# Performance work log

Hardware: AMD Instinct MI355X
Metric: run time of the kernel (lower is better)

Reference implementation:

```python
import jax, jax.numpy as jnp
import numpy as np

N = 4_194_304
Q_DIM = W_DIM = V_DIM = U_DIM = 32
LATENT = 8


def setup_inputs() -> dict:
    key = jax.random.key(0)
    k1, k2 = jax.random.split(key)
    # coords in [0,1): guarantees index+1 stays in-bounds (matches quad4d assumptions)
    uvwq = jax.random.uniform(k1, (N, 4), dtype=jnp.float32)
    grid = jax.random.normal(k2, (Q_DIM, W_DIM, V_DIM, U_DIM, LATENT), dtype=jnp.float32)
    return {"uvwq": uvwq, "grid": grid}


def reference(uvwq, grid):
    # grid: [Q, W, V, U, L]; uvwq: [N, 4] with columns (u, v, w, q) in [0,1)
    Q, W, V, U, L = grid.shape
    scale = jnp.array([U - 1, V - 1, W - 1, Q - 1], dtype=uvwq.dtype)
    idxf = uvwq * scale                      # [N,4]
    idx = idxf.astype(jnp.int32)             # floor for non-negative coords
    frac = idxf - jnp.floor(idxf)
    a = frac[:, 0:1]  # alpha (u)
    b = frac[:, 1:2]  # beta  (v)
    g = frac[:, 2:3]  # gamma (w)
    d = frac[:, 3:4]  # delta (q)
    iu, iv, iw, iq = idx[:, 0], idx[:, 1], idx[:, 2], idx[:, 3]

    def corner(oq, ow, ov, ou):
        # 16-point gather: [N, L]
        return grid[iq + oq, iw + ow, iv + ov, iu + ou]

    def lerp(x0, x1, t):
        return x0 * (1 - t) + x1 * t

    # interpolate along u (alpha)
    x000 = lerp(corner(0, 0, 0, 0), corner(0, 0, 0, 1), a)
    x001 = lerp(corner(0, 0, 1, 0), corner(0, 0, 1, 1), a)
    x010 = lerp(corner(0, 1, 0, 0), corner(0, 1, 0, 1), a)
    x011 = lerp(corner(0, 1, 1, 0), corner(0, 1, 1, 1), a)
    x100 = lerp(corner(1, 0, 0, 0), corner(1, 0, 0, 1), a)
    x101 = lerp(corner(1, 0, 1, 0), corner(1, 0, 1, 1), a)
    x110 = lerp(corner(1, 1, 0, 0), corner(1, 1, 0, 1), a)
    x111 = lerp(corner(1, 1, 1, 0), corner(1, 1, 1, 1), a)
    # along v (beta)
    x00 = lerp(x000, x001, b)
    x01 = lerp(x010, x011, b)
    x10 = lerp(x100, x101, b)
    x11 = lerp(x110, x111, b)
    # along w (gamma)
    x0 = lerp(x00, x01, g)
    x1 = lerp(x10, x11, g)
    # along q (delta)
    return lerp(x0, x1, d)  # [N, L]
```

## Files before the change

kernel.cpp:

```cpp
#include <hip/hip_runtime.h>


typedef float v4f __attribute__((ext_vector_type(4)));

#define NB   256
#define PBLK 2048
#define PT   256

__device__ __forceinline__ int bucket_of(v4f p) {
    int iw = (int)(p.z * 31.0f);
    int iq = (int)(p.w * 31.0f);
    return (iq << 3) | (iw >> 2);
}

__global__ __launch_bounds__(PT) void k_hist(const v4f* __restrict__ uvwq,
                                             int* __restrict__ hist, int n) {
    __shared__ int lh[NB];
    int t = threadIdx.x;
    lh[t] = 0;
    __syncthreads();
    int base = blockIdx.x * PBLK;
#pragma unroll
    for (int j = 0; j < 8; ++j) {
        int i = base + j * PT + t;
        if (i < n) atomicAdd(&lh[bucket_of(uvwq[i])], 1);
    }
    __syncthreads();
    atomicAdd(&hist[t], lh[t]);
}

__global__ __launch_bounds__(NB) void k_scan(const int* __restrict__ hist,
                                             int* __restrict__ cursor) {
    __shared__ int sh[NB];
    int t = threadIdx.x;
    int v = hist[t];
    sh[t] = v;
    __syncthreads();
    for (int off = 1; off < NB; off <<= 1) {
        int x = (t >= off) ? sh[t - off] : 0;
        __syncthreads();
        sh[t] += x;
        __syncthreads();
    }
    cursor[t] = sh[t] - v;
}

__global__ __launch_bounds__(PT) void k_part(const v4f* __restrict__ uvwq,
                                             int* __restrict__ cursor,
                                             v4f* __restrict__ s_uvwq,
                                             int* __restrict__ s_idx, int n) {
    __shared__ int lh[NB], lbase[NB], lrsv[NB], lcnt[NB];
    __shared__ v4f sv[PBLK];
    __shared__ int si[PBLK];
    int t = threadIdx.x;
    int base = blockIdx.x * PBLK;

    lh[t] = 0;
    lcnt[t] = 0;
    __syncthreads();

    v4f p[8];
    int key[8];
#pragma unroll
    for (int j = 0; j < 8; ++j) {
        int i = base + j * PT + t;
        if (i < n) {
            p[j] = uvwq[i];
            key[j] = bucket_of(p[j]);
            atomicAdd(&lh[key[j]], 1);
        } else key[j] = -1;
    }
    __syncthreads();

    int v = lh[t];
    lbase[t] = v;
    __syncthreads();
    for (int off = 1; off < NB; off <<= 1) {
        int x = (t >= off) ? lbase[t - off] : 0;
        __syncthreads();
        lbase[t] += x;
        __syncthreads();
    }
    int excl = lbase[t] - v;
    __syncthreads();
    lbase[t] = excl;
    lrsv[t] = atomicAdd(&cursor[t], v);
    __syncthreads();

#pragma unroll
    for (int j = 0; j < 8; ++j) {
        if (key[j] >= 0) {
            int r = lbase[key[j]] + atomicAdd(&lcnt[key[j]], 1);
            sv[r] = p[j];
            si[r] = base + j * PT + t;
        }
    }
    __syncthreads();

    int cnt = min(PBLK, n - base);
#pragma unroll
    for (int j = 0; j < 8; ++j) {
        int s = j * PT + t;
        if (s < cnt) {
            v4f q = sv[s];
            int k = bucket_of(q);
            int gp = lrsv[k] + (s - lbase[k]);
            s_uvwq[gp] = q;
            s_idx[gp] = si[s];
        }
    }
}

__global__ __launch_bounds__(256) void k_interp(const v4f* __restrict__ s_uvwq,
                                                const int* __restrict__ s_idx,
                                                const float* __restrict__ grid,
                                                v4f* __restrict__ out, int n) {
    int nb = gridDim.x;
    int b = blockIdx.x;
    int swz = (nb & 7) ? b : (b & 7) * (nb >> 3) + (b >> 3);
    int g = swz * 256 + threadIdx.x;
    if (g >= n) return;

    int oi = s_idx[g];
    v4f p = s_uvwq[g];

    float fu = p.x * 31.0f, fv = p.y * 31.0f, fw = p.z * 31.0f, fq = p.w * 31.0f;
    int iu = (int)fu, iv = (int)fv, iw = (int)fw, iq = (int)fq;
    float a = fu - (float)iu;
    float bb = fv - (float)iv;
    float gg = fw - (float)iw;
    float d = fq - (float)iq;

    const float* cellbase = grid + ((((iq * 32 + iw) * 32) + iv) * 32 + iu) * 8;

    v4f c[8][4];
#pragma unroll
    for (int k = 0; k < 8; ++k) {
        const int oq = k >> 2, ow = (k >> 1) & 1, ov = k & 1;
        const v4f* cp = (const v4f*)(cellbase + oq * 262144 + ow * 8192 + ov * 256);
        c[k][0] = cp[0];
        c[k][1] = cp[1];
        c[k][2] = cp[2];
        c[k][3] = cp[3];
    }

    float xa[8][8];
#pragma unroll
    for (int k = 0; k < 8; ++k) {
        xa[k][0] = fmaf(a, c[k][2].x - c[k][0].x, c[k][0].x);
        xa[k][1] = fmaf(a, c[k][2].y - c[k][0].y, c[k][0].y);
        xa[k][2] = fmaf(a, c[k][2].z - c[k][0].z, c[k][0].z);
        xa[k][3] = fmaf(a, c[k][2].w - c[k][0].w, c[k][0].w);
        xa[k][4] = fmaf(a, c[k][3].x - c[k][1].x, c[k][1].x);
        xa[k][5] = fmaf(a, c[k][3].y - c[k][1].y, c[k][1].y);
        xa[k][6] = fmaf(a, c[k][3].z - c[k][1].z, c[k][1].z);
        xa[k][7] = fmaf(a, c[k][3].w - c[k][1].w, c[k][1].w);
    }

    float xb[4][8];
#pragma unroll
    for (int k = 0; k < 4; ++k)
#pragma unroll
        for (int j = 0; j < 8; ++j)
            xb[k][j] = fmaf(bb, xa[2 * k + 1][j] - xa[2 * k][j], xa[2 * k][j]);

    float xg[2][8];
#pragma unroll
    for (int k = 0; k < 2; ++k)
#pragma unroll
        for (int j = 0; j < 8; ++j)
            xg[k][j] = fmaf(gg, xb[2 * k + 1][j] - xb[2 * k][j], xb[2 * k][j]);

    float r[8];
#pragma unroll
    for (int j = 0; j < 8; ++j)
        r[j] = fmaf(d, xg[1][j] - xg[0][j], xg[0][j]);

    v4f o0 = { r[0], r[1], r[2], r[3] };
    v4f o1 = { r[4], r[5], r[6], r[7] };
    __builtin_nontemporal_store(o0, &out[2 * oi + 0]);
    __builtin_nontemporal_store(o1, &out[2 * oi + 1]);
}

__global__ __launch_bounds__(256) void sg4d_direct(const v4f* __restrict__ uvwq,
                                                   const float* __restrict__ grid,
                                                   v4f* __restrict__ out, int n) {
    int i = blockIdx.x * 256 + threadIdx.x;
    if (i >= n) return;
    v4f p = uvwq[i];
    float fu = p.x * 31.0f, fv = p.y * 31.0f, fw = p.z * 31.0f, fq = p.w * 31.0f;
    int iu = (int)fu, iv = (int)fv, iw = (int)fw, iq = (int)fq;
    float a = fu - (float)iu, b = fv - (float)iv, g = fw - (float)iw, d = fq - (float)iq;
    const float* base = grid + ((((iq * 32 + iw) * 32) + iv) * 32 + iu) * 8;
    float xa[8][8];
#pragma unroll
    for (int k = 0; k < 8; ++k) {
        const int oq = k >> 2, ow = (k >> 1) & 1, ov = k & 1;
        const v4f* c = (const v4f*)(base + oq * 262144 + ow * 8192 + ov * 256);
        v4f c0 = c[0], c1 = c[1], c2 = c[2], c3 = c[3];
        xa[k][0] = fmaf(a, c2.x - c0.x, c0.x);
        xa[k][1] = fmaf(a, c2.y - c0.y, c0.y);
        xa[k][2] = fmaf(a, c2.z - c0.z, c0.z);
        xa[k][3] = fmaf(a, c2.w - c0.w, c0.w);
        xa[k][4] = fmaf(a, c3.x - c1.x, c1.x);
        xa[k][5] = fmaf(a, c3.y - c1.y, c1.y);
        xa[k][6] = fmaf(a, c3.z - c1.z, c1.z);
        xa[k][7] = fmaf(a, c3.w - c1.w, c1.w);
    }
    float xb[4][8];
#pragma unroll
    for (int k = 0; k < 4; ++k)
#pragma unroll
        for (int j = 0; j < 8; ++j)
            xb[k][j] = fmaf(b, xa[2 * k + 1][j] - xa[2 * k][j], xa[2 * k][j]);
    float xg[2][8];
#pragma unroll
    for (int k = 0; k < 2; ++k)
#pragma unroll
        for (int j = 0; j < 8; ++j)
            xg[k][j] = fmaf(g, xb[2 * k + 1][j] - xb[2 * k][j], xb[2 * k][j]);
    float r[8];
#pragma unroll
    for (int j = 0; j < 8; ++j)
        r[j] = fmaf(d, xg[1][j] - xg[0][j], xg[0][j]);
    v4f o0 = { r[0], r[1], r[2], r[3] };
    v4f o1 = { r[4], r[5], r[6], r[7] };
    __builtin_nontemporal_store(o0, &out[2 * i + 0]);
    __builtin_nontemporal_store(o1, &out[2 * i + 1]);
}

extern "C" void kernel_launch(void* const* d_in, const int* in_sizes, int n_in,
                              void* d_out, int out_size, void* d_ws, size_t ws_size,
                              hipStream_t stream) {
    const v4f*   uvwq = (const v4f*)d_in[0];
    const float* grid = (const float*)d_in[1];
    v4f*         out  = (v4f*)d_out;
    int n = in_sizes[0] / 4;

    size_t need = (size_t)n * 20 + (size_t)NB * 8 + 256;
    if (ws_size < need) {
        sg4d_direct<<<(n + 255) / 256, 256, 0, stream>>>(uvwq, grid, out, n);
        return;
    }

    char* w = (char*)d_ws;
    v4f* s_uvwq = (v4f*)w;
    int* s_idx  = (int*)(w + (size_t)n * 16);
    int* hist   = (int*)(w + (size_t)n * 20);
    int* cursor = hist + NB;

    int pblocks = (n + PBLK - 1) / PBLK;
    hipMemsetAsync(hist, 0, NB * sizeof(int), stream);
    k_hist<<<pblocks, PT, 0, stream>>>(uvwq, hist, n);
    k_scan<<<1, NB, 0, stream>>>(hist, cursor);
    k_part<<<pblocks, PT, 0, stream>>>(uvwq, cursor, s_uvwq, s_idx, n);
    k_interp<<<(n + 255) / 256, 256, 0, stream>>>(s_uvwq, s_idx, grid, out, n);
}
```

Measured before the change: 651.0 us.

## Convert grid to fp16, pack index into quantized coords, half-precision lerps

```diff
diff --git a/kernel.cpp b/kernel.cpp
--- a/kernel.cpp
+++ b/kernel.cpp
@@ -1,16 +1,34 @@
 #include <hip/hip_runtime.h>
 
 
-typedef float v4f __attribute__((ext_vector_type(4)));
+typedef float  v4f __attribute__((ext_vector_type(4)));
+typedef float  v8f __attribute__((ext_vector_type(8)));
+typedef _Float16 h8 __attribute__((ext_vector_type(8)));
 
 #define NB   256
 #define PBLK 2048
 #define PT   256
-
-__device__ __forceinline__ int bucket_of(v4f p) {
-    int iw = (int)(p.z * 31.0f);
-    int iq = (int)(p.w * 31.0f);
+#define Q26  67108864.0f
+#define S31  (31.0f / 67108864.0f)
+
+__device__ __forceinline__ uint qz(float x) {
+    uint u = (uint)(x * Q26);
+    return u > 0x3FFFFFFu ? 0x3FFFFFFu : u;
+}
+__device__ __forceinline__ int key_from_q(uint wx, uint qx) {
+    int iw = (int)((float)wx * S31);
+    int iq = (int)((float)qx * S31);
     return (iq << 3) | (iw >> 2);
+}
+
+__global__ __launch_bounds__(256) void k_cvt(const v4f* __restrict__ gf,
+                                             h8* __restrict__ gh, int nitems) {
+    int i = blockIdx.x * 256 + threadIdx.x;
+    if (i >= nitems) return;
+    v4f a = gf[2 * i], b = gf[2 * i + 1];
+    h8 h = {(_Float16)a.x, (_Float16)a.y, (_Float16)a.z, (_Float16)a.w,
+            (_Float16)b.x, (_Float16)b.y, (_Float16)b.z, (_Float16)b.w};
+    gh[i] = h;
 }
 
 __global__ __launch_bounds__(PT) void k_hist(const v4f* __restrict__ uvwq,
@@ -23,7 +41,10 @@
 #pragma unroll
     for (int j = 0; j < 8; ++j) {
         int i = base + j * PT + t;
-        if (i < n) atomicAdd(&lh[bucket_of(uvwq[i])], 1);
+        if (i < n) {
+            v4f p = uvwq[i];
+            atomicAdd(&lh[key_from_q(qz(p.z), qz(p.w))], 1);
+        }
     }
     __syncthreads();
     atomicAdd(&hist[t], lh[t]);
@@ -47,11 +68,9 @@
 
 __global__ __launch_bounds__(PT) void k_part(const v4f* __restrict__ uvwq,
                                              int* __restrict__ cursor,
-                                             v4f* __restrict__ s_uvwq,
-                                             int* __restrict__ s_idx, int n) {
+                                             uint4* __restrict__ s_rec, int n) {
     __shared__ int lh[NB], lbase[NB], lrsv[NB], lcnt[NB];
-    __shared__ v4f sv[PBLK];
-    __shared__ int si[PBLK];
+    __shared__ uint4 sv[PBLK];
     int t = threadIdx.x;
     int base = blockIdx.x * PBLK;
 
@@ -59,14 +78,20 @@
     lcnt[t] = 0;
     __syncthreads();
 
-    v4f p[8];
+    uint4 rec[8];
     int key[8];
 #pragma unroll
     for (int j = 0; j < 8; ++j) {
         int i = base + j * PT + t;
         if (i < n) {
-            p[j] = uvwq[i];
-            key[j] = bucket_of(p[j]);
+            v4f p = uvwq[i];
+            uint ux = qz(p.x), vx = qz(p.y), wx = qz(p.z), qx = qz(p.w);
+            uint idx = (uint)i;
+            rec[j].x = ux | ((idx & 63u) << 26);
+            rec[j].y = vx | (((idx >> 6) & 63u) << 26);
+            rec[j].z = wx | (((idx >> 12) & 63u) << 26);
+            rec[j].w = qx | (((idx >> 18) & 63u) << 26);
+            key[j] = key_from_q(wx, qx);
             atomicAdd(&lh[key[j]], 1);
         } else key[j] = -1;
     }
@@ -91,8 +116,7 @@
     for (int j = 0; j < 8; ++j) {
         if (key[j] >= 0) {
             int r = lbase[key[j]] + atomicAdd(&lcnt[key[j]], 1);
-            sv[r] = p[j];
-            si[r] = base + j * PT + t;
+            sv[r] = rec[j];
         }
     }
     __syncthreads();
@@ -102,18 +126,23 @@
     for (int j = 0; j < 8; ++j) {
         int s = j * PT + t;
         if (s < cnt) {
-            v4f q = sv[s];
-            int k = bucket_of(q);
-            int gp = lrsv[k] + (s - lbase[k]);
-            s_uvwq[gp] = q;
-            s_idx[gp] = si[s];
+            uint4 q = sv[s];
+            int k = key_from_q(q.z & 0x3FFFFFFu, q.w & 0x3FFFFFFu);
+            s_rec[lrsv[k] + (s - lbase[k])] = q;
         }
     }
 }
 
-__global__ __launch_bounds__(256) void k_interp(const v4f* __restrict__ s_uvwq,
-                                                const int* __restrict__ s_idx,
-                                                const float* __restrict__ grid,
+__device__ __forceinline__ h8 splat8(_Float16 x) {
+    h8 r = {x, x, x, x, x, x, x, x};
+    return r;
+}
+__device__ __forceinline__ h8 lerp8(h8 x0, h8 x1, h8 t) {
+    return x0 + t * (x1 - x0);
+}
+
+__global__ __launch_bounds__(256) void k_interp(const uint4* __restrict__ s_rec,
+                                                const _Float16* __restrict__ gridh,
                                                 v4f* __restrict__ out, int n) {
     int nb = gridDim.x;
     int b = blockIdx.x;
@@ -121,63 +150,43 @@
     int g = swz * 256 + threadIdx.x;
     if (g >= n) return;
 
-    int oi = s_idx[g];
-    v4f p = s_uvwq[g];
-
-    float fu = p.x * 31.0f, fv = p.y * 31.0f, fw = p.z * 31.0f, fq = p.w * 31.0f;
+    uint4 rec = s_rec[g];
+    float fu = (float)(rec.x & 0x3FFFFFFu) * S31;
+    float fv = (float)(rec.y & 0x3FFFFFFu) * S31;
+    float fw = (float)(rec.z & 0x3FFFFFFu) * S31;
+    float fq = (float)(rec.w & 0x3FFFFFFu) * S31;
+    int oi = (int)((rec.x >> 26) | ((rec.y >> 26) << 6) |
+                   ((rec.z >> 26) << 12) | ((rec.w >> 26) << 18));
+
     int iu = (int)fu, iv = (int)fv, iw = (int)fw, iq = (int)fq;
-    float a = fu - (float)iu;
-    float bb = fv - (float)iv;
-    float gg = fw - (float)iw;
-    float d = fq - (float)iq;
-
-    const float* cellbase = grid + ((((iq * 32 + iw) * 32) + iv) * 32 + iu) * 8;
-
-    v4f c[8][4];
+    h8 a8 = splat8((_Float16)(fu - (float)iu));
+    h8 b8 = splat8((_Float16)(fv - (float)iv));
+    h8 g8 = splat8((_Float16)(fw - (float)iw));
+    h8 d8 = splat8((_Float16)(fq - (float)iq));
+
+    const _Float16* cellh = gridh + (size_t)((((iq * 32 + iw) * 32) + iv) * 32 + iu) * 8;
+
+    h8 xa[8];
 #pragma unroll
     for (int k = 0; k < 8; ++k) {
         const int oq = k >> 2, ow = (k >> 1) & 1, ov = k & 1;
-        const v4f* cp = (const v4f*)(cellbase + oq * 262144 + ow * 8192 + ov * 256);
-        c[k][0] = cp[0];
-        c[k][1] = cp[1];
-        c[k][2] = cp[2];
-        c[k][3] = cp[3];
-    }
-
-    float xa[8][8];
-#pragma unroll
-    for (int k = 0; k < 8; ++k) {
-        xa[k][0] = fmaf(a, c[k][2].x - c[k][0].x, c[k][0].x);
-        xa[k][1] = fmaf(a, c[k][2].y - c[k][0].y, c[k][0].y);
-        xa[k][2] = fmaf(a, c[k][2].z - c[k][0].z, c[k][0].z);
-        xa[k][3] = fmaf(a, c[k][2].w - c[k][0].w, c[k][0].w);
-        xa[k][4] = fmaf(a, c[k][3].x - c[k][1].x, c[k][1].x);
-        xa[k][5] = fmaf(a, c[k][3].y - c[k][1].y, c[k][1].y);
-        xa[k][6] = fmaf(a, c[k][3].z - c[k][1].z, c[k][1].z);
-        xa[k][7] = fmaf(a, c[k][3].w - c[k][1].w, c[k][1].w);
-    }
-
-    float xb[4][8];
-#pragma unroll
-    for (int k = 0; k < 4; ++k)
-#pragma unroll
-        for (int j = 0; j < 8; ++j)
-            xb[k][j] = fmaf(bb, xa[2 * k + 1][j] - xa[2 * k][j], xa[2 * k][j]);
-
-    float xg[2][8];
-#pragma unroll
-    for (int k = 0; k < 2; ++k)
-#pragma unroll
-        for (int j = 0; j < 8; ++j)
-            xg[k][j] = fmaf(gg, xb[2 * k + 1][j] - xb[2 * k][j], xb[2 * k][j]);
-
-    float r[8];
-#pragma unroll
-    for (int j = 0; j < 8; ++j)
-        r[j] = fmaf(d, xg[1][j] - xg[0][j], xg[0][j]);
-
-    v4f o0 = { r[0], r[1], r[2], r[3] };
-    v4f o1 = { r[4], r[5], r[6], r[7] };
+        const h8* cp = (const h8*)(cellh + oq * 262144 + ow * 8192 + ov * 256);
+        h8 h0 = cp[0];
+        h8 h1 = cp[1];
+        xa[k] = lerp8(h0, h1, a8);
+    }
+
+    h8 xb[4];
+#pragma unroll
+    for (int k = 0; k < 4; ++k) xb[k] = lerp8(xa[2 * k], xa[2 * k + 1], b8);
+    h8 xg[2];
+#pragma unroll
+    for (int k = 0; k < 2; ++k) xg[k] = lerp8(xb[2 * k], xb[2 * k + 1], g8);
+    h8 xd = lerp8(xg[0], xg[1], d8);
+
+    v8f rf = __builtin_convertvector(xd, v8f);
+    v4f o0 = __builtin_shufflevector(rf, rf, 0, 1, 2, 3);
+    v4f o1 = __builtin_shufflevector(rf, rf, 4, 5, 6, 7);
     __builtin_nontemporal_store(o0, &out[2 * oi + 0]);
     __builtin_nontemporal_store(o1, &out[2 * oi + 1]);
 }
@@ -235,24 +244,27 @@
     const v4f*   uvwq = (const v4f*)d_in[0];
     const float* grid = (const float*)d_in[1];
     v4f*         out  = (v4f*)d_out;
-    int n = in_sizes[0] / 4;
-
-    size_t need = (size_t)n * 20 + (size_t)NB * 8 + 256;
+    int n  = in_sizes[0] / 4;
+    int ge = in_sizes[1];
+
+    size_t need = (size_t)n * 16 + (size_t)ge * 2 + NB * 8 + 256;
     if (ws_size < need) {
         sg4d_direct<<<(n + 255) / 256, 256, 0, stream>>>(uvwq, grid, out, n);
         return;
     }
 
     char* w = (char*)d_ws;
-    v4f* s_uvwq = (v4f*)w;
-    int* s_idx  = (int*)(w + (size_t)n * 16);
-    int* hist   = (int*)(w + (size_t)n * 20);
-    int* cursor = hist + NB;
+    uint4*     s_rec = (uint4*)w;
+    _Float16*  gridh = (_Float16*)(w + (size_t)n * 16);
+    int*       hist  = (int*)(w + (size_t)n * 16 + (size_t)ge * 2);
+    int*       cursor = hist + NB;
 
     int pblocks = (n + PBLK - 1) / PBLK;
+    int citems = ge / 8;
     hipMemsetAsync(hist, 0, NB * sizeof(int), stream);
+    k_cvt <<<(citems + 255) / 256, 256, 0, stream>>>((const v4f*)grid, (h8*)gridh, citems);
     k_hist<<<pblocks, PT, 0, stream>>>(uvwq, hist, n);
     k_scan<<<1, NB, 0, stream>>>(hist, cursor);
-    k_part<<<pblocks, PT, 0, stream>>>(uvwq, cursor, s_uvwq, s_idx, n);
-    k_interp<<<(n + 255) / 256, 256, 0, stream>>>(s_uvwq, s_idx, grid, out, n);
-}
+    k_part<<<pblocks, PT, 0, stream>>>(uvwq, cursor, s_rec, n);
+    k_interp<<<(n + 255) / 256, 256, 0, stream>>>(s_rec, gridh, out, n);
+}
```

Measured after the change: 650.8 us. About the same (-0.0%).
